# Performance work log

Measured on AMD Instinct MI355X. Metric: run time of the kernel, lower is better.

## Reference

```python
import jax, jax.numpy as jnp
import numpy as np

TOP_K = 2  # num_experts_per_tok


def setup_inputs() -> dict:
    key = jax.random.key(0)
    k1, k2, k3, k4, k5 = jax.random.split(key, 5)
    B, S, D, F, E = 2, 1024, 1024, 2048, 8
    return {
        "x": jax.random.normal(k1, (B, S, D), dtype=jnp.float32),
        "router_kernel_DE": jax.random.normal(k2, (D, E), dtype=jnp.float32) * 0.02,
        "kernel_gating_EDF": jax.random.normal(k3, (E, D, F), dtype=jnp.float32) * 0.02,
        "kernel_up_EDF": jax.random.normal(k4, (E, D, F), dtype=jnp.float32) * 0.02,
        "kernel_down_EFD": jax.random.normal(k5, (E, F, D), dtype=jnp.float32) * 0.02,
    }


def reference(x, router_kernel_DE, kernel_gating_EDF, kernel_up_EDF, kernel_down_EFD):
    E = router_kernel_DE.shape[-1]
    x = x.astype(jnp.float32)
    # --- Router ---
    logits_BSE = jnp.einsum('BSD,DE->BSE', x, router_kernel_DE)
    probs_BSE = jax.nn.softmax(logits_BSE.astype(jnp.float32), axis=-1)
    weights_BSK, indices_BSK = jax.lax.top_k(probs_BSE, TOP_K)
    norm_weights_BSK = jax.nn.softmax(weights_BSK, axis=-1)
    # scatter top-k weights into dense [B,S,E]
    one_hot_BSKE = jax.nn.one_hot(indices_BSK, num_classes=E, dtype=x.dtype)
    full_weights_BSE = jnp.sum(one_hot_BSKE * norm_weights_BSK[..., None], axis=2)
    # --- Dense-over-all-experts MoE forward ---
    gating_BSEF = jnp.einsum('BSD,EDF->BSEF', x, kernel_gating_EDF)
    act_BSEF = jax.nn.silu(gating_BSEF)
    up_BSEF = jnp.einsum('BSD,EDF->BSEF', x, kernel_up_EDF)
    fuse_BSEF = act_BSEF * up_BSEF
    down_BSED = jnp.einsum('BSEF,EFD->BSED', fuse_BSEF, kernel_down_EFD)
    out_BSD = jnp.einsum('BSED,BSE->BSD', down_BSED, full_weights_BSE)
    return out_BSD.astype(jnp.float32)
```

## Files before the change

### kernel.cpp

```cpp
#include <hip/hip_runtime.h>
#include <hip/hip_bf16.h>
#include <stdint.h>

#define T_TOK 2048
#define DIM 1024
#define FDIM 2048
#define NEXP 8
#define NSLOT 4096

typedef short bf16x8 __attribute__((ext_vector_type(8)));
typedef unsigned short u16x8 __attribute__((ext_vector_type(8)));
typedef float f32x4 __attribute__((ext_vector_type(4)));

__device__ __forceinline__ unsigned short f2bf(float f) {
  union { float f; unsigned int u; } v; v.f = f;
  unsigned int r = v.u + 0x7FFFu + ((v.u >> 16) & 1u);
  return (unsigned short)(r >> 16);
}

__device__ __forceinline__ float bf2f(unsigned short x) {
  union { unsigned int u; float f; } v; v.u = ((unsigned int)x) << 16;
  return v.f;
}

__device__ __forceinline__ void gld_lds16(const void* g, void* l) {
  __builtin_amdgcn_global_load_lds(
      (const __attribute__((address_space(1))) unsigned int*)g,
      (__attribute__((address_space(3))) unsigned int*)l, 16, 0, 0);
}

__global__ void router_kernel(const float* __restrict__ x, const float* __restrict__ rk,
                              int* __restrict__ counts, int* __restrict__ tok_e,
                              float* __restrict__ tok_w, unsigned short* __restrict__ xb) {
  int w = threadIdx.x >> 6, lane = threadIdx.x & 63;
  int t = blockIdx.x * 4 + w;
  float acc[NEXP];
#pragma unroll
  for (int e = 0; e < NEXP; ++e) acc[e] = 0.f;
  const float4* xr = (const float4*)(x + (size_t)t * DIM);
#pragma unroll
  for (int i = 0; i < 4; ++i) {
    float4 xv = xr[i * 64 + lane];
    uint2 pk;
    pk.x = ((unsigned)f2bf(xv.y) << 16) | f2bf(xv.x);
    pk.y = ((unsigned)f2bf(xv.w) << 16) | f2bf(xv.z);
    *(uint2*)(xb + (size_t)t * DIM + (i * 64 + lane) * 4) = pk;
    int d0 = (i * 64 + lane) * 4;
#pragma unroll
    for (int j = 0; j < 4; ++j) {
      const float4* rr = (const float4*)(rk + (size_t)(d0 + j) * NEXP);
      float4 r0 = rr[0], r1 = rr[1];
      float xs = (j == 0) ? xv.x : (j == 1) ? xv.y : (j == 2) ? xv.z : xv.w;
      acc[0] += xs * r0.x; acc[1] += xs * r0.y; acc[2] += xs * r0.z; acc[3] += xs * r0.w;
      acc[4] += xs * r1.x; acc[5] += xs * r1.y; acc[6] += xs * r1.z; acc[7] += xs * r1.w;
    }
  }
#pragma unroll
  for (int off = 32; off > 0; off >>= 1) {
#pragma unroll
    for (int e = 0; e < NEXP; ++e) acc[e] += __shfl_xor(acc[e], off, 64);
  }
  if (lane == 0) {
    float m = acc[0];
    for (int e = 1; e < NEXP; ++e) m = fmaxf(m, acc[e]);
    float p[NEXP], s = 0.f;
    for (int e = 0; e < NEXP; ++e) { p[e] = expf(acc[e] - m); s += p[e]; }
    float inv = 1.f / s;
    for (int e = 0; e < NEXP; ++e) p[e] *= inv;
    int i1 = 0;
    for (int e = 1; e < NEXP; ++e) if (p[e] > p[i1]) i1 = e;
    int i2 = (i1 == 0) ? 1 : 0;
    for (int e = 0; e < NEXP; ++e) if (e != i1 && p[e] > p[i2]) i2 = e;
    float e1 = expf(p[i1]), e2 = expf(p[i2]);
    float winv = 1.f / (e1 + e2);
    tok_e[t * 2] = i1; tok_e[t * 2 + 1] = i2;
    tok_w[t * 2] = e1 * winv; tok_w[t * 2 + 1] = e2 * winv;
    atomicAdd(&counts[i1], 1); atomicAdd(&counts[i2], 1);
  }
}

__global__ void assign_kernel(const int* __restrict__ tok_e, const float* __restrict__ tok_w,
                              const int* __restrict__ counts, int* __restrict__ cursor,
                              int* __restrict__ slot_token, float* __restrict__ slot_weight,
                              int* __restrict__ tok_slot) {
  int t = blockIdx.x * 256 + threadIdx.x;
  if (t >= T_TOK) return;
#pragma unroll
  for (int k = 0; k < 2; ++k) {
    int e = tok_e[t * 2 + k];
    int off = 0;
#pragma unroll
    for (int j = 0; j < NEXP; ++j) off += (j < e) ? counts[j] : 0;
    int pos = atomicAdd(&cursor[e], 1);
    int slot = off + pos;
    slot_token[slot] = t;
    slot_weight[slot] = tok_w[t * 2 + k];
    tok_slot[t * 2 + k] = slot;
  }
}

__global__ void transpose_all(const float* __restrict__ wg_f, const float* __restrict__ wu_f,
                              const float* __restrict__ wd_f, unsigned short* __restrict__ wgt,
                              unsigned short* __restrict__ wut, unsigned short* __restrict__ wdt) {
  __shared__ float lds[32][129];
  int bid = blockIdx.x, e = blockIdx.y;
  const float* in;
  unsigned short* out;
  int R, C, rb, cb;
  if (bid < 1024) {
    in = (bid < 512) ? wg_f : wu_f;
    out = (bid < 512) ? wgt : wut;
    int id = bid & 511;
    R = DIM; C = FDIM;
    cb = (id & 63) * 32; rb = (id >> 6) * 128;
  } else {
    in = wd_f; out = wdt;
    int id = bid - 1024;
    R = FDIM; C = DIM;
    cb = (id & 31) * 32; rb = (id >> 5) * 128;
  }
  size_t base = (size_t)e * (size_t)R * (size_t)C;
  int tid = threadIdx.x;
  int c4 = (tid & 7) * 4, row = tid >> 3;
#pragma unroll
  for (int it = 0; it < 4; ++it) {
    int r = row + it * 32;
    float4 v = *(const float4*)(in + base + (size_t)(rb + r) * C + cb + c4);
    lds[c4 + 0][r] = v.x; lds[c4 + 1][r] = v.y;
    lds[c4 + 2][r] = v.z; lds[c4 + 3][r] = v.w;
  }
  __syncthreads();
  int r8 = (tid & 15) * 8, c = tid >> 4;
#pragma unroll
  for (int it = 0; it < 2; ++it) {
    int cc = c + it * 16;
    uint4 v;
    v.x = ((unsigned)f2bf(lds[cc][r8 + 1]) << 16) | f2bf(lds[cc][r8 + 0]);
    v.y = ((unsigned)f2bf(lds[cc][r8 + 3]) << 16) | f2bf(lds[cc][r8 + 2]);
    v.z = ((unsigned)f2bf(lds[cc][r8 + 5]) << 16) | f2bf(lds[cc][r8 + 4]);
    v.w = ((unsigned)f2bf(lds[cc][r8 + 7]) << 16) | f2bf(lds[cc][r8 + 6]);
    *(uint4*)(out + base + (size_t)(cb + cc) * R + rb + r8) = v;
  }
}

__device__ __forceinline__ bool tile_decode(const int* counts, int ys, int& e, int& mt,
                                            int& off, int& cnt) {
  mt = ys; off = 0;
  for (e = 0; e < NEXP; ++e) {
    cnt = counts[e];
    int ntl = (cnt + 127) >> 7;
    if (mt < ntl) return true;
    mt -= ntl; off += cnt;
  }
  return false;
}

__global__ __launch_bounds__(256) void gemm_gateup(
    const unsigned short* __restrict__ xb, const unsigned short* __restrict__ wg,
    const unsigned short* __restrict__ wu, const int* __restrict__ counts,
    const int* __restrict__ slot_token, unsigned short* __restrict__ fuse) {
  int e, mt, off, cnt;
  if (!tile_decode(counts, blockIdx.y, e, mt, off, cnt)) return;
  int nt = blockIdx.x;
  __shared__ unsigned short Al[2][128 * 64];
  __shared__ unsigned short Bgl[2][64 * 64];
  __shared__ unsigned short Bul[2][64 * 64];
  int tid = threadIdx.x, w = tid >> 6, lane = tid & 63;
  int csrc = ((lane & 7) ^ (lane >> 3)) * 8;
  unsigned aoff[4];
  unsigned boff[2];
#pragma unroll
  for (int ii = 0; ii < 4; ++ii) {
    int r = (w * 4 + ii) * 8 + (lane >> 3);
    int row = mt * 128 + r;
    int tok = (row < cnt) ? slot_token[off + row] : 0;
    aoff[ii] = (unsigned)(tok * DIM + csrc);
  }
#pragma unroll
  for (int ii = 0; ii < 2; ++ii) {
    int r = (w * 2 + ii) * 8 + (lane >> 3);
    boff[ii] = (unsigned)((e * FDIM + nt * 64 + r) * DIM + csrc);
  }
  f32x4 accg[4][2] = {};
  f32x4 accu[4][2] = {};
  int wr = (w >> 1) * 64, wc = (w & 1) * 32;
  int swz = (lane & 7) << 3;
  int kof0 = ((lane >> 4) * 8) ^ swz;
  int kof1 = (32 + (lane >> 4) * 8) ^ swz;

  auto stage = [&](int buf, int k0) {
#pragma unroll
    for (int ii = 0; ii < 4; ++ii)
      gld_lds16(xb + aoff[ii] + k0, &Al[buf][(w * 4 + ii) * 512]);
#pragma unroll
    for (int ii = 0; ii < 2; ++ii) {
      gld_lds16(wg + boff[ii] + k0, &Bgl[buf][(w * 2 + ii) * 512]);
      gld_lds16(wu + boff[ii] + k0, &Bul[buf][(w * 2 + ii) * 512]);
    }
  };
  auto compute = [&](int buf) {
#pragma unroll
    for (int kk = 0; kk < 2; ++kk) {
      int kof = kk ? kof1 : kof0;
      bf16x8 af[4], bg[2], bu[2];
#pragma unroll
      for (int q = 0; q < 4; ++q)
        af[q] = *(const bf16x8*)&Al[buf][(wr + q * 16 + (lane & 15)) * 64 + kof];
#pragma unroll
      for (int q = 0; q < 2; ++q) {
        bg[q] = *(const bf16x8*)&Bgl[buf][(wc + q * 16 + (lane & 15)) * 64 + kof];
        bu[q] = *(const bf16x8*)&Bul[buf][(wc + q * 16 + (lane & 15)) * 64 + kof];
      }
#pragma unroll
      for (int m4 = 0; m4 < 4; ++m4) {
#pragma unroll
        for (int n4 = 0; n4 < 2; ++n4) {
          accg[m4][n4] = __builtin_amdgcn_mfma_f32_16x16x32_bf16(af[m4], bg[n4], accg[m4][n4], 0, 0, 0);
          accu[m4][n4] = __builtin_amdgcn_mfma_f32_16x16x32_bf16(af[m4], bu[n4], accu[m4][n4], 0, 0, 0);
        }
      }
    }
  };

  stage(0, 0);
  asm volatile("s_waitcnt vmcnt(0)" ::: "memory");
  __builtin_amdgcn_s_barrier();
  int cb = 0;
  for (int k0 = 0; k0 < DIM; k0 += 64) {
    if (k0 + 64 < DIM) stage(cb ^ 1, k0 + 64);
    __builtin_amdgcn_sched_barrier(0);
    compute(cb);
    __builtin_amdgcn_sched_barrier(0);
    asm volatile("s_waitcnt vmcnt(0)" ::: "memory");
    __builtin_amdgcn_s_barrier();
    cb ^= 1;
  }

#pragma unroll
  for (int m4 = 0; m4 < 4; ++m4) {
#pragma unroll
    for (int n4 = 0; n4 < 2; ++n4) {
      f32x4 g = accg[m4][n4], u = accu[m4][n4];
#pragma unroll
      for (int j = 0; j < 4; ++j) {
        int r = wr + m4 * 16 + (lane >> 4) * 4 + j;
        int row = mt * 128 + r;
        if (row < cnt) {
          float gv = g[j];
          float val = gv / (1.f + expf(-gv)) * u[j];
          int f = nt * 64 + wc + n4 * 16 + (lane & 15);
          fuse[(size_t)(off + row) * FDIM + f] = f2bf(val);
        }
      }
    }
  }
}

__global__ __launch_bounds__(256) void gemm_down(
    const unsigned short* __restrict__ fuse, const unsigned short* __restrict__ wd,
    const int* __restrict__ counts, const float* __restrict__ slot_weight,
    unsigned short* __restrict__ part4) {
  int e, mt, off, cnt;
  if (!tile_decode(counts, blockIdx.y, e, mt, off, cnt)) return;
  int nt = blockIdx.x;
  int z = blockIdx.z;
  int kbase = z * (FDIM / 4);
  __shared__ unsigned short Al[128 * 64];
  __shared__ unsigned short Bl[2][128 * 64];
  int tid = threadIdx.x, w = tid >> 6, lane = tid & 63;
  int csrc = ((lane & 7) ^ (lane >> 3)) * 8;
  unsigned aoff[4];
  unsigned boff[4];
#pragma unroll
  for (int ii = 0; ii < 4; ++ii) {
    int r = (w * 4 + ii) * 8 + (lane >> 3);
    int row = mt * 128 + r;
    int grow = (row < cnt) ? (off + row) : off;
    aoff[ii] = (unsigned)(grow * FDIM + kbase + csrc);
    boff[ii] = (unsigned)((e * DIM + nt * 128 + r) * FDIM + kbase + csrc);
  }
  f32x4 acc[4][4] = {};
  int wr = (w >> 1) * 64, wc = (w & 1) * 64;
  int swz = (lane & 7) << 3;
  int kof0 = ((lane >> 4) * 8) ^ swz;
  int kof1 = (32 + (lane >> 4) * 8) ^ swz;

  auto stage_A = [&](int k0) {
#pragma unroll
    for (int ii = 0; ii < 4; ++ii)
      gld_lds16(fuse + aoff[ii] + k0, &Al[(w * 4 + ii) * 512]);
  };
  auto stage_B = [&](int buf, int k0) {
#pragma unroll
    for (int ii = 0; ii < 4; ++ii)
      gld_lds16(wd + boff[ii] + k0, &Bl[buf][(w * 4 + ii) * 512]);
  };
  auto compute = [&](int buf) {
#pragma unroll
    for (int kk = 0; kk < 2; ++kk) {
      int kof = kk ? kof1 : kof0;
      bf16x8 af[4], bfr[4];
#pragma unroll
      for (int q = 0; q < 4; ++q) {
        af[q] = *(const bf16x8*)&Al[(wr + q * 16 + (lane & 15)) * 64 + kof];
        bfr[q] = *(const bf16x8*)&Bl[buf][(wc + q * 16 + (lane & 15)) * 64 + kof];
      }
#pragma unroll
      for (int m4 = 0; m4 < 4; ++m4) {
#pragma unroll
        for (int n4 = 0; n4 < 4; ++n4) {
          acc[m4][n4] = __builtin_amdgcn_mfma_f32_16x16x32_bf16(af[m4], bfr[n4], acc[m4][n4], 0, 0, 0);
        }
      }
    }
  };

  stage_B(0, 0);
  stage_A(0);
  asm volatile("s_waitcnt vmcnt(0)" ::: "memory");
  __builtin_amdgcn_s_barrier();
  int cb = 0;
  for (int t = 0; t < 8; ++t) {
    if (t < 7) {
      stage_B(cb ^ 1, (t + 1) * 64);
      __builtin_amdgcn_sched_barrier(0);
      asm volatile("s_waitcnt vmcnt(4)" ::: "memory");
    } else {
      asm volatile("s_waitcnt vmcnt(0)" ::: "memory");
    }
    __builtin_amdgcn_s_barrier();
    __builtin_amdgcn_sched_barrier(0);
    compute(cb);
    __builtin_amdgcn_sched_barrier(0);
    __builtin_amdgcn_s_barrier();
    if (t < 7) stage_A((t + 1) * 64);
    cb ^= 1;
  }

#pragma unroll
  for (int m4 = 0; m4 < 4; ++m4) {
#pragma unroll
    for (int j = 0; j < 4; ++j) {
      int r = wr + m4 * 16 + (lane >> 4) * 4 + j;
      int row = mt * 128 + r;
      if (row < cnt) {
        float wgt = slot_weight[off + row];
#pragma unroll
        for (int n4 = 0; n4 < 4; ++n4) {
          int d = nt * 128 + wc + n4 * 16 + (lane & 15);
          part4[((size_t)z * NSLOT + off + row) * DIM + d] = f2bf(acc[m4][n4][j] * wgt);
        }
      }
    }
  }
}

__global__ void combine_kernel(const unsigned short* __restrict__ part4,
                               const int* __restrict__ tok_slot, float* __restrict__ out) {
  int i = blockIdx.x * 256 + threadIdx.x;
  int t = i >> 7;
  int c = i & 127;
  int s0 = tok_slot[t * 2], s1 = tok_slot[t * 2 + 1];
  const u16x8* base = (const u16x8*)part4;
  float o[8];
#pragma unroll
  for (int j = 0; j < 8; ++j) o[j] = 0.f;
#pragma unroll
  for (int z = 0; z < 4; ++z) {
    u16x8 a = base[((size_t)z * NSLOT + s0) * (DIM / 8) + c];
    u16x8 b = base[((size_t)z * NSLOT + s1) * (DIM / 8) + c];
#pragma unroll
    for (int j = 0; j < 8; ++j) o[j] += bf2f(a[j]) + bf2f(b[j]);
  }
  float4* dst = (float4*)(out + (size_t)t * DIM + c * 8);
  dst[0] = make_float4(o[0], o[1], o[2], o[3]);
  dst[1] = make_float4(o[4], o[5], o[6], o[7]);
}

extern "C" void kernel_launch(void* const* d_in, const int* in_sizes, int n_in,
                              void* d_out, int out_size, void* d_ws, size_t ws_size,
                              hipStream_t stream) {
  (void)in_sizes; (void)n_in; (void)out_size;
  const float* x    = (const float*)d_in[0];
  const float* rk   = (const float*)d_in[1];
  const float* wg_f = (const float*)d_in[2];
  const float* wu_f = (const float*)d_in[3];
  const float* wd_f = (const float*)d_in[4];
  float* out = (float*)d_out;

  char* ws = (char*)d_ws;
  size_t o_xb   = 0;
  size_t o_wg   = o_xb + (size_t)T_TOK * DIM * 2;
  size_t o_wu   = o_wg + (size_t)NEXP * FDIM * DIM * 2;
  size_t o_wd   = o_wu + (size_t)NEXP * FDIM * DIM * 2;
  size_t o_fuse = o_wd + (size_t)NEXP * DIM * FDIM * 2;
  size_t o_meta = o_fuse + (size_t)NSLOT * FDIM * 2;
  size_t o_counts = o_meta;
  size_t o_cursor = o_counts + 32;
  size_t o_tok_e  = o_cursor + 32;
  size_t o_tok_w  = o_tok_e + (size_t)T_TOK * 2 * 4;
  size_t o_tok_s  = o_tok_w + (size_t)T_TOK * 2 * 4;
  size_t o_st     = o_tok_s + (size_t)T_TOK * 2 * 4;
  size_t o_sw     = o_st + (size_t)NSLOT * 4;
  size_t need     = o_sw + (size_t)NSLOT * 4;
  if (ws_size < need) return;

  unsigned short* xb    = (unsigned short*)(ws + o_xb);
  unsigned short* wgt   = (unsigned short*)(ws + o_wg);
  unsigned short* wut   = (unsigned short*)(ws + o_wu);
  unsigned short* wdt   = (unsigned short*)(ws + o_wd);
  unsigned short* fuse  = (unsigned short*)(ws + o_fuse);
  unsigned short* part4 = (unsigned short*)(ws + o_wg);
  int* counts          = (int*)(ws + o_counts);
  int* cursor          = (int*)(ws + o_cursor);
  int* tok_e           = (int*)(ws + o_tok_e);
  float* tok_w         = (float*)(ws + o_tok_w);
  int* tok_slot        = (int*)(ws + o_tok_s);
  int* slot_token      = (int*)(ws + o_st);
  float* slot_weight   = (float*)(ws + o_sw);

  hipMemsetAsync(ws + o_counts, 0, 64, stream);
  router_kernel<<<T_TOK / 4, 256, 0, stream>>>(x, rk, counts, tok_e, tok_w, xb);
  assign_kernel<<<T_TOK / 256, 256, 0, stream>>>(tok_e, tok_w, counts, cursor,
                                                 slot_token, slot_weight, tok_slot);
  transpose_all<<<dim3(1536, NEXP), 256, 0, stream>>>(wg_f, wu_f, wd_f, wgt, wut, wdt);
  gemm_gateup<<<dim3(FDIM / 64, 40, 1), 256, 0, stream>>>(xb, wgt, wut, counts,
                                                          slot_token, fuse);
  gemm_down<<<dim3(DIM / 128, 40, 4), 256, 0, stream>>>(fuse, wdt, counts,
                                                        slot_weight, part4);
  combine_kernel<<<(T_TOK * DIM / 8) / 256, 256, 0, stream>>>(part4, tok_slot, out);
}
```

Baseline: 243.2 us.

## Fuse fp32 weight transpose and bf16 conversion into expert GEMM B-tile loads

Drops the separate transpose_all kernel, which read all fp32 expert weights and wrote transposed bf16 copies. Each GEMM now loads fp32 weights from global memory into registers, converts them to bf16 and writes them into a swizzled LDS layout during the k-loop. gemm_down also gets a double-buffered A tile, and part4 moves to its own workspace region. The goal is to avoid writing and re-reading roughly 200 MB of weights. The cost is that each weight tile is now fetched as fp32 by every token tile of the same expert, instead of as bf16. The loads are also strided scalar accesses across rows, so coalescing is weaker.

```diff
diff --git a/kernel.cpp b/kernel.cpp
--- a/kernel.cpp
+++ b/kernel.cpp
@@ -99,50 +99,6 @@
   }
 }
 
-__global__ void transpose_all(const float* __restrict__ wg_f, const float* __restrict__ wu_f,
-                              const float* __restrict__ wd_f, unsigned short* __restrict__ wgt,
-                              unsigned short* __restrict__ wut, unsigned short* __restrict__ wdt) {
-  __shared__ float lds[32][129];
-  int bid = blockIdx.x, e = blockIdx.y;
-  const float* in;
-  unsigned short* out;
-  int R, C, rb, cb;
-  if (bid < 1024) {
-    in = (bid < 512) ? wg_f : wu_f;
-    out = (bid < 512) ? wgt : wut;
-    int id = bid & 511;
-    R = DIM; C = FDIM;
-    cb = (id & 63) * 32; rb = (id >> 6) * 128;
-  } else {
-    in = wd_f; out = wdt;
-    int id = bid - 1024;
-    R = FDIM; C = DIM;
-    cb = (id & 31) * 32; rb = (id >> 5) * 128;
-  }
-  size_t base = (size_t)e * (size_t)R * (size_t)C;
-  int tid = threadIdx.x;
-  int c4 = (tid & 7) * 4, row = tid >> 3;
-#pragma unroll
-  for (int it = 0; it < 4; ++it) {
-    int r = row + it * 32;
-    float4 v = *(const float4*)(in + base + (size_t)(rb + r) * C + cb + c4);
-    lds[c4 + 0][r] = v.x; lds[c4 + 1][r] = v.y;
-    lds[c4 + 2][r] = v.z; lds[c4 + 3][r] = v.w;
-  }
-  __syncthreads();
-  int r8 = (tid & 15) * 8, c = tid >> 4;
-#pragma unroll
-  for (int it = 0; it < 2; ++it) {
-    int cc = c + it * 16;
-    uint4 v;
-    v.x = ((unsigned)f2bf(lds[cc][r8 + 1]) << 16) | f2bf(lds[cc][r8 + 0]);
-    v.y = ((unsigned)f2bf(lds[cc][r8 + 3]) << 16) | f2bf(lds[cc][r8 + 2]);
-    v.z = ((unsigned)f2bf(lds[cc][r8 + 5]) << 16) | f2bf(lds[cc][r8 + 4]);
-    v.w = ((unsigned)f2bf(lds[cc][r8 + 7]) << 16) | f2bf(lds[cc][r8 + 6]);
-    *(uint4*)(out + base + (size_t)(cb + cc) * R + rb + r8) = v;
-  }
-}
-
 __device__ __forceinline__ bool tile_decode(const int* counts, int ys, int& e, int& mt,
                                             int& off, int& cnt) {
   mt = ys; off = 0;
@@ -156,8 +112,8 @@
 }
 
 __global__ __launch_bounds__(256) void gemm_gateup(
-    const unsigned short* __restrict__ xb, const unsigned short* __restrict__ wg,
-    const unsigned short* __restrict__ wu, const int* __restrict__ counts,
+    const unsigned short* __restrict__ xb, const float* __restrict__ wgf,
+    const float* __restrict__ wuf, const int* __restrict__ counts,
     const int* __restrict__ slot_token, unsigned short* __restrict__ fuse) {
   int e, mt, off, cnt;
   if (!tile_decode(counts, blockIdx.y, e, mt, off, cnt)) return;
@@ -168,7 +124,6 @@
   int tid = threadIdx.x, w = tid >> 6, lane = tid & 63;
   int csrc = ((lane & 7) ^ (lane >> 3)) * 8;
   unsigned aoff[4];
-  unsigned boff[2];
 #pragma unroll
   for (int ii = 0; ii < 4; ++ii) {
     int r = (w * 4 + ii) * 8 + (lane >> 3);
@@ -176,11 +131,9 @@
     int tok = (row < cnt) ? slot_token[off + row] : 0;
     aoff[ii] = (unsigned)(tok * DIM + csrc);
   }
-#pragma unroll
-  for (int ii = 0; ii < 2; ++ii) {
-    int r = (w * 2 + ii) * 8 + (lane >> 3);
-    boff[ii] = (unsigned)((e * FDIM + nt * 64 + r) * DIM + csrc);
-  }
+  int bf = tid >> 2, dsel = tid & 3;
+  const float* wg_base = wgf + (size_t)e * DIM * FDIM + (size_t)(nt * 64 + bf);
+  const float* wu_base = wuf + (size_t)e * DIM * FDIM + (size_t)(nt * 64 + bf);
   f32x4 accg[4][2] = {};
   f32x4 accu[4][2] = {};
   int wr = (w >> 1) * 64, wc = (w & 1) * 32;
@@ -188,15 +141,36 @@
   int kof0 = ((lane >> 4) * 8) ^ swz;
   int kof1 = (32 + (lane >> 4) * 8) ^ swz;
 
-  auto stage = [&](int buf, int k0) {
+  float bgv[16], buv[16];
+  auto loadB = [&](int k0) {
+#pragma unroll
+    for (int it = 0; it < 4; ++it) {
+#pragma unroll
+      for (int i = 0; i < 4; ++i) {
+        int d = k0 + dsel * 4 + it * 16 + i;
+        bgv[it * 4 + i] = wg_base[(size_t)d * FDIM];
+        buv[it * 4 + i] = wu_base[(size_t)d * FDIM];
+      }
+    }
+  };
+  auto writeB = [&](int buf) {
+#pragma unroll
+    for (int it = 0; it < 4; ++it) {
+      int dl = dsel * 4 + it * 16;
+      int o16 = bf * 64 + (((dl >> 3) ^ (bf & 7)) * 8) + (dl & 7);
+      uint2 g, u;
+      g.x = ((unsigned)f2bf(bgv[it * 4 + 1]) << 16) | f2bf(bgv[it * 4 + 0]);
+      g.y = ((unsigned)f2bf(bgv[it * 4 + 3]) << 16) | f2bf(bgv[it * 4 + 2]);
+      u.x = ((unsigned)f2bf(buv[it * 4 + 1]) << 16) | f2bf(buv[it * 4 + 0]);
+      u.y = ((unsigned)f2bf(buv[it * 4 + 3]) << 16) | f2bf(buv[it * 4 + 2]);
+      *(uint2*)&Bgl[buf][o16] = g;
+      *(uint2*)&Bul[buf][o16] = u;
+    }
+  };
+  auto stage_A = [&](int buf, int k0) {
 #pragma unroll
     for (int ii = 0; ii < 4; ++ii)
       gld_lds16(xb + aoff[ii] + k0, &Al[buf][(w * 4 + ii) * 512]);
-#pragma unroll
-    for (int ii = 0; ii < 2; ++ii) {
-      gld_lds16(wg + boff[ii] + k0, &Bgl[buf][(w * 2 + ii) * 512]);
-      gld_lds16(wu + boff[ii] + k0, &Bul[buf][(w * 2 + ii) * 512]);
-    }
   };
   auto compute = [&](int buf) {
 #pragma unroll
@@ -222,16 +196,22 @@
     }
   };
 
-  stage(0, 0);
-  asm volatile("s_waitcnt vmcnt(0)" ::: "memory");
+  loadB(0);
+  stage_A(0, 0);
+  writeB(0);
+  asm volatile("s_waitcnt vmcnt(0) lgkmcnt(0)" ::: "memory");
   __builtin_amdgcn_s_barrier();
   int cb = 0;
-  for (int k0 = 0; k0 < DIM; k0 += 64) {
-    if (k0 + 64 < DIM) stage(cb ^ 1, k0 + 64);
+  for (int t = 0; t < 16; ++t) {
+    if (t < 15) {
+      loadB((t + 1) * 64);
+      stage_A(cb ^ 1, (t + 1) * 64);
+    }
     __builtin_amdgcn_sched_barrier(0);
     compute(cb);
+    if (t < 15) writeB(cb ^ 1);
     __builtin_amdgcn_sched_barrier(0);
-    asm volatile("s_waitcnt vmcnt(0)" ::: "memory");
+    asm volatile("s_waitcnt vmcnt(0) lgkmcnt(0)" ::: "memory");
     __builtin_amdgcn_s_barrier();
     cb ^= 1;
   }
@@ -257,7 +237,7 @@
 }
 
 __global__ __launch_bounds__(256) void gemm_down(
-    const unsigned short* __restrict__ fuse, const unsigned short* __restrict__ wd,
+    const unsigned short* __restrict__ fuse, const float* __restrict__ wdf,
     const int* __restrict__ counts, const float* __restrict__ slot_weight,
     unsigned short* __restrict__ part4) {
   int e, mt, off, cnt;
@@ -265,35 +245,52 @@
   int nt = blockIdx.x;
   int z = blockIdx.z;
   int kbase = z * (FDIM / 4);
-  __shared__ unsigned short Al[128 * 64];
+  __shared__ unsigned short Al[2][128 * 64];
   __shared__ unsigned short Bl[2][128 * 64];
   int tid = threadIdx.x, w = tid >> 6, lane = tid & 63;
   int csrc = ((lane & 7) ^ (lane >> 3)) * 8;
   unsigned aoff[4];
-  unsigned boff[4];
 #pragma unroll
   for (int ii = 0; ii < 4; ++ii) {
     int r = (w * 4 + ii) * 8 + (lane >> 3);
     int row = mt * 128 + r;
     int grow = (row < cnt) ? (off + row) : off;
     aoff[ii] = (unsigned)(grow * FDIM + kbase + csrc);
-    boff[ii] = (unsigned)((e * DIM + nt * 128 + r) * FDIM + kbase + csrc);
-  }
+  }
+  int bd = tid >> 1, fsel = tid & 1;
+  const float* wd_base = wdf + (size_t)e * FDIM * DIM + (size_t)(nt * 128 + bd);
   f32x4 acc[4][4] = {};
   int wr = (w >> 1) * 64, wc = (w & 1) * 64;
   int swz = (lane & 7) << 3;
   int kof0 = ((lane >> 4) * 8) ^ swz;
   int kof1 = (32 + (lane >> 4) * 8) ^ swz;
 
-  auto stage_A = [&](int k0) {
+  float bv[32];
+  auto loadB = [&](int k0) {
+#pragma unroll
+    for (int it = 0; it < 8; ++it) {
+#pragma unroll
+      for (int i = 0; i < 4; ++i) {
+        int f = kbase + k0 + fsel * 4 + it * 8 + i;
+        bv[it * 4 + i] = wd_base[(size_t)f * DIM];
+      }
+    }
+  };
+  auto writeB = [&](int buf) {
+#pragma unroll
+    for (int it = 0; it < 8; ++it) {
+      int fl = fsel * 4 + it * 8;
+      int o16 = bd * 64 + (((fl >> 3) ^ (bd & 7)) * 8) + (fl & 7);
+      uint2 v;
+      v.x = ((unsigned)f2bf(bv[it * 4 + 1]) << 16) | f2bf(bv[it * 4 + 0]);
+      v.y = ((unsigned)f2bf(bv[it * 4 + 3]) << 16) | f2bf(bv[it * 4 + 2]);
+      *(uint2*)&Bl[buf][o16] = v;
+    }
+  };
+  auto stage_A = [&](int buf, int k0) {
 #pragma unroll
     for (int ii = 0; ii < 4; ++ii)
-      gld_lds16(fuse + aoff[ii] + k0, &Al[(w * 4 + ii) * 512]);
-  };
-  auto stage_B = [&](int buf, int k0) {
-#pragma unroll
-    for (int ii = 0; ii < 4; ++ii)
-      gld_lds16(wd + boff[ii] + k0, &Bl[buf][(w * 4 + ii) * 512]);
+      gld_lds16(fuse + aoff[ii] + k0, &Al[buf][(w * 4 + ii) * 512]);
   };
   auto compute = [&](int buf) {
 #pragma unroll
@@ -302,7 +299,7 @@
       bf16x8 af[4], bfr[4];
 #pragma unroll
       for (int q = 0; q < 4; ++q) {
-        af[q] = *(const bf16x8*)&Al[(wr + q * 16 + (lane & 15)) * 64 + kof];
+        af[q] = *(const bf16x8*)&Al[buf][(wr + q * 16 + (lane & 15)) * 64 + kof];
         bfr[q] = *(const bf16x8*)&Bl[buf][(wc + q * 16 + (lane & 15)) * 64 + kof];
       }
 #pragma unroll
@@ -315,25 +312,23 @@
     }
   };
 
-  stage_B(0, 0);
-  stage_A(0);
-  asm volatile("s_waitcnt vmcnt(0)" ::: "memory");
+  loadB(0);
+  stage_A(0, 0);
+  writeB(0);
+  asm volatile("s_waitcnt vmcnt(0) lgkmcnt(0)" ::: "memory");
   __builtin_amdgcn_s_barrier();
   int cb = 0;
   for (int t = 0; t < 8; ++t) {
     if (t < 7) {
-      stage_B(cb ^ 1, (t + 1) * 64);
-      __builtin_amdgcn_sched_barrier(0);
-      asm volatile("s_waitcnt vmcnt(4)" ::: "memory");
-    } else {
-      asm volatile("s_waitcnt vmcnt(0)" ::: "memory");
-    }
-    __builtin_amdgcn_s_barrier();
+      loadB((t + 1) * 64);
+      stage_A(cb ^ 1, (t + 1) * 64);
+    }
     __builtin_amdgcn_sched_barrier(0);
     compute(cb);
+    if (t < 7) writeB(cb ^ 1);
     __builtin_amdgcn_sched_barrier(0);
+    asm volatile("s_waitcnt vmcnt(0) lgkmcnt(0)" ::: "memory");
     __builtin_amdgcn_s_barrier();
-    if (t < 7) stage_A((t + 1) * 64);
     cb ^= 1;
   }
 
@@ -390,11 +385,9 @@
 
   char* ws = (char*)d_ws;
   size_t o_xb   = 0;
-  size_t o_wg   = o_xb + (size_t)T_TOK * DIM * 2;
-  size_t o_wu   = o_wg + (size_t)NEXP * FDIM * DIM * 2;
-  size_t o_wd   = o_wu + (size_t)NEXP * FDIM * DIM * 2;
-  size_t o_fuse = o_wd + (size_t)NEXP * DIM * FDIM * 2;
-  size_t o_meta = o_fuse + (size_t)NSLOT * FDIM * 2;
+  size_t o_fuse = o_xb + (size_t)T_TOK * DIM * 2;
+  size_t o_part = o_fuse + (size_t)NSLOT * FDIM * 2;
+  size_t o_meta = o_part + (size_t)4 * NSLOT * DIM * 2;
   size_t o_counts = o_meta;
   size_t o_cursor = o_counts + 32;
   size_t o_tok_e  = o_cursor + 32;
@@ -406,11 +399,8 @@
   if (ws_size < need) return;
 
   unsigned short* xb    = (unsigned short*)(ws + o_xb);
-  unsigned short* wgt   = (unsigned short*)(ws + o_wg);
-  unsigned short* wut   = (unsigned short*)(ws + o_wu);
-  unsigned short* wdt   = (unsigned short*)(ws + o_wd);
   unsigned short* fuse  = (unsigned short*)(ws + o_fuse);
-  unsigned short* part4 = (unsigned short*)(ws + o_wg);
+  unsigned short* part4 = (unsigned short*)(ws + o_part);
   int* counts          = (int*)(ws + o_counts);
   int* cursor          = (int*)(ws + o_cursor);
   int* tok_e           = (int*)(ws + o_tok_e);
@@ -423,10 +413,9 @@
   router_kernel<<<T_TOK / 4, 256, 0, stream>>>(x, rk, counts, tok_e, tok_w, xb);
   assign_kernel<<<T_TOK / 256, 256, 0, stream>>>(tok_e, tok_w, counts, cursor,
                                                  slot_token, slot_weight, tok_slot);
-  transpose_all<<<dim3(1536, NEXP), 256, 0, stream>>>(wg_f, wu_f, wd_f, wgt, wut, wdt);
-  gemm_gateup<<<dim3(FDIM / 64, 40, 1), 256, 0, stream>>>(xb, wgt, wut, counts,
+  gemm_gateup<<<dim3(FDIM / 64, 40, 1), 256, 0, stream>>>(xb, wg_f, wu_f, counts,
                                                           slot_token, fuse);
-  gemm_down<<<dim3(DIM / 128, 40, 4), 256, 0, stream>>>(fuse, wdt, counts,
+  gemm_down<<<dim3(DIM / 128, 40, 4), 256, 0, stream>>>(fuse, wd_f, counts,
                                                         slot_weight, part4);
   combine_kernel<<<(T_TOK * DIM / 8) / 256, 256, 0, stream>>>(part4, tok_slot, out);
 }
```

Measured after the change: 280.0 us. 15.1% more time.

## Halve gate/up K-tile to 32 and add partial-wait double-buffer pipeline

Applied to the files above, without the earlier changes.

Shrinks the gate/up GEMM K step from 64 to 32, halving LDS use per buffer and changing the XOR swizzle to fit 32-wide rows. The loop now issues the next stage's loads, waits only for the previous stage (vmcnt(4)), and puts a barrier on each side of compute. The aim is to raise occupancy through the smaller LDS footprint and to keep loads in flight during compute. In exchange it runs twice as many iterations and barriers per tile, and there is less MFMA work to hide each wait.

```diff
diff --git a/kernel.cpp b/kernel.cpp
--- a/kernel.cpp
+++ b/kernel.cpp
@@ -162,62 +162,52 @@
   int e, mt, off, cnt;
   if (!tile_decode(counts, blockIdx.y, e, mt, off, cnt)) return;
   int nt = blockIdx.x;
-  __shared__ unsigned short Al[2][128 * 64];
-  __shared__ unsigned short Bgl[2][64 * 64];
-  __shared__ unsigned short Bul[2][64 * 64];
+  __shared__ unsigned short Al[2][128 * 32];
+  __shared__ unsigned short Bgl[2][64 * 32];
+  __shared__ unsigned short Bul[2][64 * 32];
   int tid = threadIdx.x, w = tid >> 6, lane = tid & 63;
-  int csrc = ((lane & 7) ^ (lane >> 3)) * 8;
-  unsigned aoff[4];
-  unsigned boff[2];
-#pragma unroll
-  for (int ii = 0; ii < 4; ++ii) {
-    int r = (w * 4 + ii) * 8 + (lane >> 3);
+  int csrc = ((lane & 3) ^ ((lane >> 3) & 3)) * 8;
+  unsigned aoff[2];
+  unsigned boff;
+#pragma unroll
+  for (int ii = 0; ii < 2; ++ii) {
+    int r = (w * 2 + ii) * 16 + (lane >> 2);
     int row = mt * 128 + r;
     int tok = (row < cnt) ? slot_token[off + row] : 0;
     aoff[ii] = (unsigned)(tok * DIM + csrc);
   }
-#pragma unroll
-  for (int ii = 0; ii < 2; ++ii) {
-    int r = (w * 2 + ii) * 8 + (lane >> 3);
-    boff[ii] = (unsigned)((e * FDIM + nt * 64 + r) * DIM + csrc);
+  {
+    int r = w * 16 + (lane >> 2);
+    boff = (unsigned)((e * FDIM + nt * 64 + r) * DIM + csrc);
   }
   f32x4 accg[4][2] = {};
   f32x4 accu[4][2] = {};
   int wr = (w >> 1) * 64, wc = (w & 1) * 32;
-  int swz = (lane & 7) << 3;
-  int kof0 = ((lane >> 4) * 8) ^ swz;
-  int kof1 = (32 + (lane >> 4) * 8) ^ swz;
+  int kof = ((lane >> 4) ^ ((lane >> 1) & 3)) * 8;
 
   auto stage = [&](int buf, int k0) {
 #pragma unroll
-    for (int ii = 0; ii < 4; ++ii)
-      gld_lds16(xb + aoff[ii] + k0, &Al[buf][(w * 4 + ii) * 512]);
-#pragma unroll
-    for (int ii = 0; ii < 2; ++ii) {
-      gld_lds16(wg + boff[ii] + k0, &Bgl[buf][(w * 2 + ii) * 512]);
-      gld_lds16(wu + boff[ii] + k0, &Bul[buf][(w * 2 + ii) * 512]);
-    }
+    for (int ii = 0; ii < 2; ++ii)
+      gld_lds16(xb + aoff[ii] + k0, &Al[buf][(w * 2 + ii) * 512]);
+    gld_lds16(wg + boff + k0, &Bgl[buf][w * 512]);
+    gld_lds16(wu + boff + k0, &Bul[buf][w * 512]);
   };
   auto compute = [&](int buf) {
-#pragma unroll
-    for (int kk = 0; kk < 2; ++kk) {
-      int kof = kk ? kof1 : kof0;
-      bf16x8 af[4], bg[2], bu[2];
-#pragma unroll
-      for (int q = 0; q < 4; ++q)
-        af[q] = *(const bf16x8*)&Al[buf][(wr + q * 16 + (lane & 15)) * 64 + kof];
-#pragma unroll
-      for (int q = 0; q < 2; ++q) {
-        bg[q] = *(const bf16x8*)&Bgl[buf][(wc + q * 16 + (lane & 15)) * 64 + kof];
-        bu[q] = *(const bf16x8*)&Bul[buf][(wc + q * 16 + (lane & 15)) * 64 + kof];
-      }
-#pragma unroll
-      for (int m4 = 0; m4 < 4; ++m4) {
-#pragma unroll
-        for (int n4 = 0; n4 < 2; ++n4) {
-          accg[m4][n4] = __builtin_amdgcn_mfma_f32_16x16x32_bf16(af[m4], bg[n4], accg[m4][n4], 0, 0, 0);
-          accu[m4][n4] = __builtin_amdgcn_mfma_f32_16x16x32_bf16(af[m4], bu[n4], accu[m4][n4], 0, 0, 0);
-        }
+    bf16x8 af[4], bg[2], bu[2];
+#pragma unroll
+    for (int q = 0; q < 4; ++q)
+      af[q] = *(const bf16x8*)&Al[buf][(wr + q * 16 + (lane & 15)) * 32 + kof];
+#pragma unroll
+    for (int q = 0; q < 2; ++q) {
+      bg[q] = *(const bf16x8*)&Bgl[buf][(wc + q * 16 + (lane & 15)) * 32 + kof];
+      bu[q] = *(const bf16x8*)&Bul[buf][(wc + q * 16 + (lane & 15)) * 32 + kof];
+    }
+#pragma unroll
+    for (int m4 = 0; m4 < 4; ++m4) {
+#pragma unroll
+      for (int n4 = 0; n4 < 2; ++n4) {
+        accg[m4][n4] = __builtin_amdgcn_mfma_f32_16x16x32_bf16(af[m4], bg[n4], accg[m4][n4], 0, 0, 0);
+        accu[m4][n4] = __builtin_amdgcn_mfma_f32_16x16x32_bf16(af[m4], bu[n4], accu[m4][n4], 0, 0, 0);
       }
     }
   };
@@ -226,12 +216,18 @@
   asm volatile("s_waitcnt vmcnt(0)" ::: "memory");
   __builtin_amdgcn_s_barrier();
   int cb = 0;
-  for (int k0 = 0; k0 < DIM; k0 += 64) {
-    if (k0 + 64 < DIM) stage(cb ^ 1, k0 + 64);
+  for (int t = 0; t < 32; ++t) {
+    if (t < 31) {
+      stage(cb ^ 1, (t + 1) * 32);
+      __builtin_amdgcn_sched_barrier(0);
+      asm volatile("s_waitcnt vmcnt(4)" ::: "memory");
+    } else {
+      asm volatile("s_waitcnt vmcnt(0)" ::: "memory");
+    }
+    __builtin_amdgcn_s_barrier();
     __builtin_amdgcn_sched_barrier(0);
     compute(cb);
     __builtin_amdgcn_sched_barrier(0);
-    asm volatile("s_waitcnt vmcnt(0)" ::: "memory");
     __builtin_amdgcn_s_barrier();
     cb ^= 1;
   }
```

New measurement: 247.7 us. Within noise of the previous version (+1.8%).
